# Performance work log

Measured on AMD Instinct MI355X. Metric: run time of the kernel, lower is better.

## Reference

```python
import jax, jax.numpy as jnp
import numpy as np
import math

DIM, HEADS, COMPRESS = 2048, 16, 8
HEAD_DIM = DIM // HEADS          # 128
HALF = HEAD_DIM // 2             # 64 (Q/K head dim after low-rank up-proj)
LATENT = DIM // COMPRESS         # 256
B, S = 2, 2048


def setup_inputs() -> dict:
    key = jax.random.key(0)
    ks = jax.random.split(key, 7)
    sc = lambda fan_in: 1.0 / math.sqrt(fan_in)
    return {
        "x": jax.random.normal(ks[0], (B, S, DIM), jnp.float32),
        "wq_d": jax.random.normal(ks[1], (DIM, LATENT), jnp.float32) * sc(DIM),
        "wkv_d": jax.random.normal(ks[2], (DIM, LATENT), jnp.float32) * sc(DIM),
        "wq_u": jax.random.normal(ks[3], (LATENT, HEADS * HALF), jnp.float32) * sc(LATENT),
        "wk_u": jax.random.normal(ks[4], (LATENT, HEADS * HALF), jnp.float32) * sc(LATENT),
        "wv_u": jax.random.normal(ks[5], (LATENT, DIM), jnp.float32) * sc(LATENT),
        "wo": jax.random.normal(ks[6], (DIM, DIM), jnp.float32) * sc(DIM),
    }


def _rope_tables(seq_len):
    # LlamaRotaryEmbedding with dim = HALF
    inv_freq = 1.0 / (10000.0 ** (jnp.arange(0, HALF, 2, dtype=jnp.float32) / HALF))  # [HALF//2]
    t = jnp.arange(seq_len, dtype=jnp.float32)
    freqs = t[:, None] * inv_freq[None, :]          # [S, HALF//2]
    emb = jnp.concatenate([freqs, freqs], axis=-1)  # [S, HALF]
    cos = jnp.cos(emb)[None, :, None, :]            # [1, S, 1, HALF]
    sin = jnp.sin(emb)[None, :, None, :]
    return cos, sin


def _rotate_half(x):
    x1, x2 = jnp.split(x, 2, axis=-1)
    return jnp.concatenate([-x2, x1], axis=-1)


def reference(x, wq_d, wkv_d, wq_u, wk_u, wv_u, wo):
    b, s, d = x.shape
    q_latent = x @ wq_d                      # [B,S,LATENT]
    kv_latent = x @ wkv_d                    # [B,S,LATENT]
    q = (q_latent @ wq_u).reshape(b, s, HEADS, HALF)
    k = (kv_latent @ wk_u).reshape(b, s, HEADS, HALF)
    v = (kv_latent @ wv_u).reshape(b, s, HEADS, HEAD_DIM)

    cos, sin = _rope_tables(s)
    q = q * cos + _rotate_half(q) * sin
    k = k * cos + _rotate_half(k) * sin

    scale = 1.0 / math.sqrt(HALF)
    attn = jnp.einsum("bqhd,bkhd->bhqk", q, k) * scale   # [B,H,S,S] (no mask, as in source)
    attn = jax.nn.softmax(attn, axis=-1)
    out = jnp.einsum("bhqk,bkhd->bqhd", attn, v)         # [B,S,H,HEAD_DIM]
    out = out.reshape(b, s, d)
    return out @ wo
```

## Files before the change

### kernel.cpp

```cpp
#include <hip/hip_runtime.h>
#include <stdint.h>

typedef unsigned short u16;
typedef __attribute__((ext_vector_type(8))) short bf16x8;
typedef __attribute__((ext_vector_type(4))) float f32x4;
typedef __attribute__((ext_vector_type(4))) unsigned short u16x4;

#define DIM 2048
#define HEADS 16
#define HEAD_DIM 128
#define HALF 64
#define LATENT 256
#define BATCH 2
#define SEQ 2048
#define TOK (BATCH*SEQ)

#if defined(__has_builtin)
#if __has_builtin(__builtin_amdgcn_exp2f)
#define EXP2F(x) __builtin_amdgcn_exp2f(x)
#endif
#endif
#ifndef EXP2F
#define EXP2F(x) exp2f(x)
#endif

#define SCALE_C 0.18033688011112042f

__device__ __forceinline__ u16 f2bf(float f) {
  uint32_t u = __float_as_uint(f);
  u += 0x7fff + ((u >> 16) & 1);
  return (u16)(u >> 16);
}

__device__ __forceinline__ f32x4 mfma16(bf16x8 a, bf16x8 b, f32x4 c) {
  return __builtin_amdgcn_mfma_f32_16x16x32_bf16(a, b, c, 0, 0, 0);
}

__device__ __forceinline__ void async_copy16(const void* g, void* l) {
  __builtin_amdgcn_global_load_lds(
      (const __attribute__((address_space(1))) void*)g,
      (__attribute__((address_space(3))) void*)l, 16, 0, 0);
}

__global__ void prep_k(const float* __restrict__ wq_d, const float* __restrict__ wkv_d,
                       const float* __restrict__ wq_u, const float* __restrict__ wk_u,
                       const float* __restrict__ wv_u, const float* __restrict__ wo,
                       u16* __restrict__ wdT, u16* __restrict__ wquT, u16* __restrict__ wkuT,
                       u16* __restrict__ wvuT, u16* __restrict__ woT,
                       float* __restrict__ ct, float* __restrict__ st) {
  __shared__ float tile[32][33];
  const int f = blockIdx.x;
  const int tx = threadIdx.x, ty = threadIdx.y;

  const float* in = nullptr;
  u16* out = nullptr;
  int N = 0, row_off = 0, out_ld = 0, bx = 0, by = 0;

  if (f < 1024) {
    int z = f >> 9, r = f & 511;
    bx = r & 7; by = r >> 3;
    in = z ? wkv_d : wq_d; out = wdT; row_off = z * 256; N = 256; out_ld = 2048;
  } else if (f < 1536) {
    int r = f - 1024; int z = r >> 8; r &= 255;
    bx = r & 31; by = r >> 5;
    in = z ? wk_u : wq_u; out = z ? wkuT : wquT; row_off = 0; N = 1024; out_ld = 256;
  } else if (f < 2048) {
    int r = f - 1536;
    bx = r & 63; by = r >> 6;
    in = wv_u; out = wvuT; row_off = 0; N = 2048; out_ld = 256;
  } else if (f < 6144) {
    int r = f - 2048;
    bx = r & 63; by = r >> 6;
    in = wo; out = woT; row_off = 0; N = 2048; out_ld = 2048;
  } else {
    int t = (f - 6144) * 256 + ty * 32 + tx;
    int i = t & 31, s = t >> 5;
    float invf = expf(-(float)i * 0.28782313662425575f);
    float a = (float)s * invf;
    ct[t] = cosf(a);
    st[t] = sinf(a);
    return;
  }
  int k0 = by * 32, n0 = bx * 32;
  #pragma unroll
  for (int j = 0; j < 32; j += 8)
    tile[ty + j][tx] = in[(size_t)(k0 + ty + j) * N + n0 + tx];
  __syncthreads();
  #pragma unroll
  for (int j = 0; j < 32; j += 8)
    out[(size_t)(n0 + ty + j + row_off) * out_ld + k0 + tx] = f2bf(tile[tx][ty + j]);
}

template<int NS, int OUTF32>
__global__ void combine_k(const float* __restrict__ p, void* __restrict__ out, int n4, int slab4) {
  int t = blockIdx.x * 256 + threadIdx.x;
  if (t >= n4) return;
  float4 a = ((const float4*)p)[t];
  #pragma unroll
  for (int s = 1; s < NS; ++s) {
    float4 b = ((const float4*)p)[t + (size_t)s * slab4];
    a.x += b.x; a.y += b.y; a.z += b.z; a.w += b.w;
  }
  if (OUTF32) ((float4*)out)[t] = a;
  else { u16x4 o = { f2bf(a.x), f2bf(a.y), f2bf(a.z), f2bf(a.w) };
         *(u16x4*)((u16*)out + (size_t)t * 4) = o; }
}

__global__ __launch_bounds__(256)
void gemm_lat(const float* __restrict__ A, int lda, const u16* __restrict__ BT, int ldb,
              float* __restrict__ Cv, int M, int N, int K) {
  __shared__ __align__(16) u16 As[128 * 32];
  __shared__ __align__(16) u16 Bs[128 * 32];
  const int tid = threadIdx.x;
  const int lane = tid & 63;
  const int wid = tid >> 6;
  const int z = blockIdx.z;
  int koff = z * K;
  const int nb = gridDim.x * gridDim.y;
  int f = blockIdx.x + gridDim.x * blockIdx.y;
  f = (f & 7) * (nb >> 3) + (f >> 3);
  const int m0 = (f / gridDim.x) * 128;
  const int n0 = (f % gridDim.x) * 128;
  const int wr = wid >> 1, wc = wid & 1;
  const int l15 = lane & 15, lg = lane >> 4;
  const int rA = lane >> 2;
  const int kqL = (lane & 3) * 8;
  const int kqS = ((((lane & 3) - ((lane >> 3) & 3)) & 3)) * 8;
  const int sWr = (((lane & 3) + ((lane >> 3) & 3)) & 3) * 8;
  const int rsw = (l15 >> 1) & 3;

  f32x4 acc[4][4] = {};
  const int nk = K / 32;
  for (int kt = 0; kt < nk; ++kt) {
    const int k0 = koff + kt * 32;
    #pragma unroll
    for (int c = 0; c < 2; ++c) {
      int ca = wid * 2 + c;
      const float* ga = A + (size_t)(m0 + ca * 16 + rA) * lda + k0 + kqL;
      float4 v0 = *(const float4*)ga;
      float4 v1 = *(const float4*)(ga + 4);
      union { u16 h[8]; bf16x8 v; } pk;
      pk.h[0] = f2bf(v0.x); pk.h[1] = f2bf(v0.y); pk.h[2] = f2bf(v0.z); pk.h[3] = f2bf(v0.w);
      pk.h[4] = f2bf(v1.x); pk.h[5] = f2bf(v1.y); pk.h[6] = f2bf(v1.z); pk.h[7] = f2bf(v1.w);
      *(bf16x8*)&As[ca * 512 + rA * 32 + sWr] = pk.v;
      const u16* gb = BT + (size_t)(n0 + ca * 16 + rA) * ldb + k0 + kqS;
      async_copy16(gb, &Bs[ca * 512]);
    }
    __syncthreads();
    bf16x8 af[4], bfr[4];
    const int slot = ((lg + rsw) & 3) * 8;
    #pragma unroll
    for (int i = 0; i < 4; ++i) {
      af[i]  = *(const bf16x8*)&As[(wr * 64 + i * 16 + l15) * 32 + slot];
      bfr[i] = *(const bf16x8*)&Bs[(wc * 64 + i * 16 + l15) * 32 + slot];
    }
    #pragma unroll
    for (int i = 0; i < 4; ++i)
      #pragma unroll
      for (int j = 0; j < 4; ++j)
        acc[i][j] = mfma16(af[i], bfr[j], acc[i][j]);
    __syncthreads();
  }
  #pragma unroll
  for (int i = 0; i < 4; ++i) {
    #pragma unroll
    for (int j = 0; j < 4; ++j) {
      int row = m0 + wr * 64 + i * 16 + lg * 4;
      int col = n0 + wc * 64 + j * 16 + l15;
      #pragma unroll
      for (int r = 0; r < 4; ++r)
        Cv[(size_t)z * M * N + (size_t)(row + r) * N + col] = acc[i][j][r];
    }
  }
}

__global__ __launch_bounds__(256)
void gemm_wo(const u16* __restrict__ A, const u16* __restrict__ BT,
             float* __restrict__ C) {
  __shared__ __align__(16) u16 As[3][128 * 32];
  __shared__ __align__(16) u16 Bs[3][128 * 32];
  const int tid = threadIdx.x, lane = tid & 63, wid = tid >> 6;
  const int nb = gridDim.x * gridDim.y;
  int f = blockIdx.x + gridDim.x * blockIdx.y;
  f = (f & 7) * (nb >> 3) + (f >> 3);
  const int m0 = (f / gridDim.x) * 128;
  const int n0 = (f % gridDim.x) * 128;
  const int wr = wid >> 1, wc = wid & 1;
  const int l15 = lane & 15, lg = lane >> 4;
  const int rA = lane >> 2;
  const int kqS = ((((lane & 3) - ((lane >> 3) & 3)) & 3)) * 8;
  const int rsw = (l15 >> 1) & 3;

  f32x4 acc[4][4] = {};

  auto stage = [&](u16* AsD, u16* BsD, int k0) {
    #pragma unroll
    for (int c = 0; c < 2; ++c) {
      int ca = wid * 2 + c;
      async_copy16(A + (size_t)(m0 + ca * 16 + rA) * DIM + k0 + kqS, AsD + ca * 512);
      async_copy16(BT + (size_t)(n0 + ca * 16 + rA) * DIM + k0 + kqS, BsD + ca * 512);
    }
  };
  auto compute = [&](const u16* AsP, const u16* BsP) {
    bf16x8 af[4], bfr[4];
    const int slot = ((lg + rsw) & 3) * 8;
    #pragma unroll
    for (int i = 0; i < 4; ++i) {
      af[i]  = *(const bf16x8*)&AsP[(wr * 64 + i * 16 + l15) * 32 + slot];
      bfr[i] = *(const bf16x8*)&BsP[(wc * 64 + i * 16 + l15) * 32 + slot];
    }
    __builtin_amdgcn_s_setprio(1);
    #pragma unroll
    for (int i = 0; i < 4; ++i)
      #pragma unroll
      for (int j = 0; j < 4; ++j)
        acc[i][j] = mfma16(af[i], bfr[j], acc[i][j]);
    __builtin_amdgcn_s_setprio(0);
  };

#define WAIT4 asm volatile("s_waitcnt vmcnt(4)" ::: "memory")
#define WAIT0 asm volatile("s_waitcnt vmcnt(0)" ::: "memory")
#define BAR   __builtin_amdgcn_s_barrier()

  stage(As[0], Bs[0], 0);
  stage(As[1], Bs[1], 32);
  WAIT4; BAR;
  int t = 0;
  for (int i = 0; i < 20; ++i) {
    stage(As[2], Bs[2], (t + 2) * 32); compute(As[0], Bs[0]); WAIT4; BAR;
    stage(As[0], Bs[0], (t + 3) * 32); compute(As[1], Bs[1]); WAIT4; BAR;
    stage(As[1], Bs[1], (t + 4) * 32); compute(As[2], Bs[2]); WAIT4; BAR;
    t += 3;
  }
  stage(As[2], Bs[2], 62 * 32); compute(As[0], Bs[0]); WAIT4; BAR;
  stage(As[0], Bs[0], 63 * 32); compute(As[1], Bs[1]); WAIT4; BAR;
  compute(As[2], Bs[2]); WAIT0; BAR;
  compute(As[0], Bs[0]);

#undef WAIT4
#undef WAIT0
#undef BAR

  #pragma unroll
  for (int i = 0; i < 4; ++i) {
    #pragma unroll
    for (int j = 0; j < 4; ++j) {
      int row = m0 + wr * 64 + i * 16 + lg * 4;
      int col = n0 + wc * 64 + j * 16 + l15;
      #pragma unroll
      for (int r = 0; r < 4; ++r)
        C[(size_t)(row + r) * DIM + col] = acc[i][j][r];
    }
  }
}

__global__ __launch_bounds__(256)
void upproj_k(const u16* __restrict__ A,
              const u16* __restrict__ wquT, const u16* __restrict__ wkuT,
              const u16* __restrict__ wvuT,
              u16* __restrict__ qb, u16* __restrict__ kb, u16* __restrict__ vT,
              const float* __restrict__ ct, const float* __restrict__ st) {
  __shared__ __align__(16) u16 As[128 * 32];
  __shared__ __align__(16) u16 Bs[128 * 32];
  const int tid = threadIdx.x;
  const int lane = tid & 63;
  const int wid = tid >> 6;
  int f = blockIdx.x;
  f = (f & 7) * 128 + (f >> 3);
  const u16* BT; u16* out; int N, a_off, seg, r;
  if (f < 256)      { seg = 0; r = f;       BT = wquT; out = qb; N = 1024; a_off = 0; }
  else if (f < 512) { seg = 1; r = f - 256; BT = wkuT; out = kb; N = 1024; a_off = 256; }
  else              { seg = 2; r = f - 512; BT = wvuT; out = vT; N = 2048; a_off = 256; }
  const int gx = (seg == 2) ? 16 : 8;
  const int m0 = (r / gx) * 128;
  const int n0 = (r % gx) * 128;
  const int wr = wid >> 1, wc = wid & 1;
  const int l15 = lane & 15, lg = lane >> 4;
  const int rA = lane >> 2;
  const int kqS = ((((lane & 3) - ((lane >> 3) & 3)) & 3)) * 8;
  const int rsw = (l15 >> 1) & 3;

  f32x4 acc[4][4] = {};
  for (int kt = 0; kt < LATENT / 32; ++kt) {
    const int k0 = kt * 32;
    #pragma unroll
    for (int c = 0; c < 2; ++c) {
      int ca = wid * 2 + c;
      async_copy16(A + (size_t)(m0 + ca * 16 + rA) * 512 + a_off + k0 + kqS, &As[ca * 512]);
      async_copy16(BT + (size_t)(n0 + ca * 16 + rA) * LATENT + k0 + kqS, &Bs[ca * 512]);
    }
    __syncthreads();
    bf16x8 af[4], bfr[4];
    const int slot = ((lg + rsw) & 3) * 8;
    #pragma unroll
    for (int i = 0; i < 4; ++i) {
      af[i]  = *(const bf16x8*)&As[(wr * 64 + i * 16 + l15) * 32 + slot];
      bfr[i] = *(const bf16x8*)&Bs[(wc * 64 + i * 16 + l15) * 32 + slot];
    }
    #pragma unroll
    for (int i = 0; i < 4; ++i)
      #pragma unroll
      for (int j = 0; j < 4; ++j)
        acc[i][j] = mfma16(af[i], bfr[j], acc[i][j]);
    __syncthreads();
  }

  if (seg <= 1) {
    const float qs = seg ? 1.0f : SCALE_C;
    #pragma unroll
    for (int i = 0; i < 4; ++i) {
      int rowb = m0 + wr * 64 + i * 16 + lg * 4;
      #pragma unroll
      for (int j = 0; j < 2; ++j) {
        int ii = j * 16 + l15;
        int colb = n0 + wc * 64;
        #pragma unroll
        for (int r2 = 0; r2 < 4; ++r2) {
          int s = (rowb + r2) & (SEQ - 1);
          float c = ct[s * 32 + ii], sn = st[s * 32 + ii];
          float x1 = acc[i][j][r2], x2 = acc[i][j + 2][r2];
          out[(size_t)(rowb + r2) * N + colb + ii]      = f2bf((x1 * c - x2 * sn) * qs);
          out[(size_t)(rowb + r2) * N + colb + ii + 32] = f2bf((x2 * c + x1 * sn) * qs);
        }
      }
    }
  } else {
    const int bb = m0 >> 11;
    #pragma unroll
    for (int i = 0; i < 4; ++i) {
      int rowb = m0 + wr * 64 + i * 16 + lg * 4;
      int s = rowb & (SEQ - 1);
      int pbase = (s & ~31) + (((s & 15) >> 2) << 3) + (((s >> 4) & 1) << 2);
      #pragma unroll
      for (int j = 0; j < 4; ++j) {
        int c = n0 + wc * 64 + j * 16 + l15;
        u16x4 ov = { f2bf(acc[i][j][0]), f2bf(acc[i][j][1]),
                     f2bf(acc[i][j][2]), f2bf(acc[i][j][3]) };
        *(u16x4*)&out[(size_t)bb * SEQ * DIM + (size_t)c * SEQ + pbase] = ov;
      }
    }
  }
}

#define KVB 64
__global__ __launch_bounds__(256, 2)
void attn_kernel(const u16* __restrict__ Q, const u16* __restrict__ Kb,
                 const u16* __restrict__ VT, u16* __restrict__ O) {
  __shared__ __align__(16) u16 Ks[3][KVB * 64];
  __shared__ __align__(16) u16 Vs[3][HEAD_DIM * KVB];

  const int tid = threadIdx.x, lane = tid & 63, wid = tid >> 6;
  int fl = blockIdx.x + 16 * (blockIdx.y + 16 * blockIdx.z);
  fl = (fl & 7) * 64 + (fl >> 3);
  const int q0 = (fl & 15) * 128;
  const int h = (fl >> 4) & 15;
  const int b = fl >> 8;
  const int l15 = lane & 15, lg = lane >> 4;

  const u16* kbp = Kb + (size_t)(b * SEQ) * (HEADS * HALF) + h * HALF;
  const u16* vtb = VT + (size_t)b * SEQ * DIM + (size_t)(h * HEAD_DIM) * SEQ;

  bf16x8 qf[2][2];
  #pragma unroll
  for (int m = 0; m < 2; ++m)
    #pragma unroll
    for (int ks = 0; ks < 2; ++ks)
      qf[m][ks] = *(const bf16x8*)&Q[(size_t)(b * SEQ + q0 + wid * 32 + m * 16 + l15) * (HEADS * HALF)
                                     + h * HALF + ks * 32 + lg * 8];

  f32x4 o[2][8] = {};
  float l_part[2] = {0.f, 0.f};

  const int row8 = lane >> 3;
  const int colB = ((lane & 7) ^ row8) * 16;

  auto stage = [&](u16* KsD, u16* VsD, int kv0) {
    #pragma unroll
    for (int i = 0; i < 2; ++i) {
      int c = wid * 2 + i;
      const u16* src = kbp + (size_t)(kv0 + c * 8 + row8) * (HEADS * HALF) + (colB >> 1);
      async_copy16(src, KsD + c * 512);
    }
    #pragma unroll
    for (int i = 0; i < 4; ++i) {
      int c = wid * 4 + i;
      const u16* src = vtb + (size_t)(c * 8 + row8) * SEQ + kv0 + (colB >> 1);
      async_copy16(src, VsD + c * 512);
    }
  };

  auto compute = [&](const u16* KsP, const u16* VsP) {
    const char* KsB = (const char*)KsP;
    const char* VsB = (const char*)VsP;
    const int kswz = (l15 & 7) << 4;
    bf16x8 kf[2][4];
    #pragma unroll
    for (int ks = 0; ks < 2; ++ks)
      #pragma unroll
      for (int nf = 0; nf < 4; ++nf)
        kf[ks][nf] = *(const bf16x8*)(KsB + (nf * 16 + l15) * 128 + ((ks * 64 + lg * 16) ^ kswz));
    f32x4 s[2][4] = {};
    __builtin_amdgcn_s_setprio(1);
    #pragma unroll
    for (int ks = 0; ks < 2; ++ks)
      #pragma unroll
      for (int nf = 0; nf < 4; ++nf) {
        s[0][nf] = mfma16(kf[ks][nf], qf[0][ks], s[0][nf]);
        s[1][nf] = mfma16(kf[ks][nf], qf[1][ks], s[1][nf]);
      }
    __builtin_amdgcn_s_setprio(0);
    #pragma unroll
    for (int ks2 = 0; ks2 < 2; ++ks2) {
      bf16x8 vf[8];
      #pragma unroll
      for (int db = 0; db < 8; ++db) {
        int row = db * 16 + l15;
        vf[db] = *(const bf16x8*)(VsB + row * 128 + ((ks2 * 64 + lg * 16) ^ ((row & 7) << 4)));
      }
      bf16x8 pa[2];
      #pragma unroll
      for (int m = 0; m < 2; ++m) {
        float p[8];
        #pragma unroll
        for (int nf2 = 0; nf2 < 2; ++nf2)
          #pragma unroll
          for (int r = 0; r < 4; ++r) {
            float v = EXP2F(s[m][ks2 * 2 + nf2][r]);
            p[nf2 * 4 + r] = v;
            l_part[m] += v;
          }
        union { uint32_t u[4]; bf16x8 v8; } pk;
        asm("v_cvt_pk_bf16_f32 %0, %1, %2" : "=v"(pk.u[0]) : "v"(p[0]), "v"(p[1]));
        asm("v_cvt_pk_bf16_f32 %0, %1, %2" : "=v"(pk.u[1]) : "v"(p[2]), "v"(p[3]));
        asm("v_cvt_pk_bf16_f32 %0, %1, %2" : "=v"(pk.u[2]) : "v"(p[4]), "v"(p[5]));
        asm("v_cvt_pk_bf16_f32 %0, %1, %2" : "=v"(pk.u[3]) : "v"(p[6]), "v"(p[7]));
        pa[m] = pk.v8;
      }
      __builtin_amdgcn_s_setprio(1);
      #pragma unroll
      for (int db = 0; db < 8; ++db) {
        o[0][db] = mfma16(pa[0], vf[db], o[0][db]);
        o[1][db] = mfma16(pa[1], vf[db], o[1][db]);
      }
      __builtin_amdgcn_s_setprio(0);
    }
  };

#define WAIT6 asm volatile("s_waitcnt vmcnt(6)" ::: "memory")
#define WAIT0 asm volatile("s_waitcnt vmcnt(0)" ::: "memory")
#define BAR   __builtin_amdgcn_s_barrier()

  stage(Ks[0], Vs[0], 0);
  stage(Ks[1], Vs[1], KVB);
  WAIT6; BAR;
  int t = 0;
  for (int i = 0; i < 10; ++i) {
    stage(Ks[2], Vs[2], (t + 2) * KVB); compute(Ks[0], Vs[0]); WAIT6; BAR;
    stage(Ks[0], Vs[0], (t + 3) * KVB); compute(Ks[1], Vs[1]); WAIT6; BAR;
    stage(Ks[1], Vs[1], (t + 4) * KVB); compute(Ks[2], Vs[2]); WAIT6; BAR;
    t += 3;
  }
  compute(Ks[0], Vs[0]); WAIT0; BAR;
  compute(Ks[1], Vs[1]);

#undef WAIT6
#undef WAIT0
#undef BAR

  #pragma unroll
  for (int m = 0; m < 2; ++m) {
    float l = l_part[m];
    l += __shfl_xor(l, 16);
    l += __shfl_xor(l, 32);
    float inv[4];
    #pragma unroll
    for (int r = 0; r < 4; ++r)
      inv[r] = 1.0f / __shfl(l, lg * 4 + r);
    #pragma unroll
    for (int db = 0; db < 8; ++db)
      #pragma unroll
      for (int r = 0; r < 4; ++r) {
        int row = q0 + wid * 32 + m * 16 + lg * 4 + r;
        O[(size_t)(b * SEQ + row) * DIM + h * HEAD_DIM + db * 16 + l15] = f2bf(o[m][db][r] * inv[r]);
      }
  }
}

extern "C" void kernel_launch(void* const* d_in, const int* in_sizes, int n_in,
                              void* d_out, int out_size, void* d_ws, size_t ws_size,
                              hipStream_t stream) {
  const float* x     = (const float*)d_in[0];
  const float* wq_d  = (const float*)d_in[1];
  const float* wkv_d = (const float*)d_in[2];
  const float* wq_u  = (const float*)d_in[3];
  const float* wk_u  = (const float*)d_in[4];
  const float* wv_u  = (const float*)d_in[5];
  const float* wo    = (const float*)d_in[6];

  char* ws = (char*)d_ws;
  size_t off = 0;
  auto alloc = [&](size_t bytes) -> void* {
    void* p = ws + off;
    off += (bytes + 255) & ~(size_t)255;
    return p;
  };
  u16* wdT    = (u16*)alloc((size_t)512 * DIM * 2);
  u16* wquT   = (u16*)alloc((size_t)1024 * LATENT * 2);
  u16* wkuT   = (u16*)alloc((size_t)1024 * LATENT * 2);
  u16* wvuT   = (u16*)alloc((size_t)DIM * LATENT * 2);
  u16* woT    = (u16*)alloc((size_t)DIM * DIM * 2);
  u16* lat    = (u16*)alloc((size_t)TOK * 512 * 2);
  float* latP = (float*)alloc((size_t)4 * TOK * 512 * 4);
  u16* qb     = (u16*)alloc((size_t)TOK * 1024 * 2);
  u16* kb     = (u16*)alloc((size_t)TOK * 1024 * 2);
  u16* vT     = (u16*)alloc((size_t)TOK * DIM * 2);
  u16* ao     = (u16*)alloc((size_t)TOK * DIM * 2);
  float* ct   = (float*)alloc((size_t)SEQ * 32 * 4);
  float* st   = (float*)alloc((size_t)SEQ * 32 * 4);
  (void)in_sizes; (void)n_in; (void)out_size; (void)ws_size;

  prep_k<<<dim3(6400), dim3(32, 8), 0, stream>>>(wq_d, wkv_d, wq_u, wk_u, wv_u, wo,
                                                 wdT, wquT, wkuT, wvuT, woT, ct, st);

  gemm_lat<<<dim3(4, 32, 4), 256, 0, stream>>>(x, DIM, wdT, DIM, latP, TOK, 512, 512);
  combine_k<4, 0><<<(TOK * 512 / 4 + 255) / 256, 256, 0, stream>>>(latP, lat, TOK * 512 / 4, TOK * 512 / 4);

  upproj_k<<<dim3(1024), 256, 0, stream>>>(lat, wquT, wkuT, wvuT, qb, kb, vT, ct, st);

  attn_kernel<<<dim3(SEQ / 128, HEADS, BATCH), 256, 0, stream>>>(qb, kb, vT, ao);

  gemm_wo<<<dim3(16, 32), 256, 0, stream>>>(ao, woT, (float*)d_out);
}
```

Measured before the change: 157.6 us.

## Store split-K latent partials in bf16 and triple-buffer upproj K loop

The split-K latent GEMM now writes its partial sums as bf16 instead of fp32, and the combine kernel reads and sums bf16 partials eight elements at a time. This halves partial-buffer traffic but adds an extra rounding step before the final sum. The up-projection kernel also gets a 3-stage async LDS pipeline with vmcnt waits, barriers and MFMA priority raising, so global loads overlap compute instead of syncing twice per K step.

```diff
diff --git a/kernel.cpp b/kernel.cpp
--- a/kernel.cpp
+++ b/kernel.cpp
@@ -3,6 +3,7 @@
 
 typedef unsigned short u16;
 typedef __attribute__((ext_vector_type(8))) short bf16x8;
+typedef __attribute__((ext_vector_type(8))) unsigned short u16x8;
 typedef __attribute__((ext_vector_type(4))) float f32x4;
 typedef __attribute__((ext_vector_type(4))) unsigned short u16x4;
 
@@ -30,6 +31,10 @@
   uint32_t u = __float_as_uint(f);
   u += 0x7fff + ((u >> 16) & 1);
   return (u16)(u >> 16);
+}
+
+__device__ __forceinline__ float bf2f(u16 h) {
+  return __uint_as_float((uint32_t)h << 16);
 }
 
 __device__ __forceinline__ f32x4 mfma16(bf16x8 a, bf16x8 b, f32x4 c) {
@@ -91,24 +96,27 @@
     out[(size_t)(n0 + ty + j + row_off) * out_ld + k0 + tx] = f2bf(tile[tx][ty + j]);
 }
 
-template<int NS, int OUTF32>
-__global__ void combine_k(const float* __restrict__ p, void* __restrict__ out, int n4, int slab4) {
+__global__ void combine_bf(const u16* __restrict__ p, u16* __restrict__ out,
+                           int n8, size_t slab) {
   int t = blockIdx.x * 256 + threadIdx.x;
-  if (t >= n4) return;
-  float4 a = ((const float4*)p)[t];
-  #pragma unroll
-  for (int s = 1; s < NS; ++s) {
-    float4 b = ((const float4*)p)[t + (size_t)s * slab4];
-    a.x += b.x; a.y += b.y; a.z += b.z; a.w += b.w;
-  }
-  if (OUTF32) ((float4*)out)[t] = a;
-  else { u16x4 o = { f2bf(a.x), f2bf(a.y), f2bf(a.z), f2bf(a.w) };
-         *(u16x4*)((u16*)out + (size_t)t * 4) = o; }
+  if (t >= n8) return;
+  size_t base = (size_t)t * 8;
+  float a[8] = {};
+  #pragma unroll
+  for (int s = 0; s < 4; ++s) {
+    u16x8 v = *(const u16x8*)&p[base + s * slab];
+    #pragma unroll
+    for (int e = 0; e < 8; ++e) a[e] += bf2f(v[e]);
+  }
+  u16x8 o;
+  #pragma unroll
+  for (int e = 0; e < 8; ++e) o[e] = f2bf(a[e]);
+  *(u16x8*)&out[base] = o;
 }
 
 __global__ __launch_bounds__(256)
 void gemm_lat(const float* __restrict__ A, int lda, const u16* __restrict__ BT, int ldb,
-              float* __restrict__ Cv, int M, int N, int K) {
+              u16* __restrict__ Cv, int M, int N, int K) {
   __shared__ __align__(16) u16 As[128 * 32];
   __shared__ __align__(16) u16 Bs[128 * 32];
   const int tid = threadIdx.x;
@@ -169,7 +177,7 @@
       int col = n0 + wc * 64 + j * 16 + l15;
       #pragma unroll
       for (int r = 0; r < 4; ++r)
-        Cv[(size_t)z * M * N + (size_t)(row + r) * N + col] = acc[i][j][r];
+        Cv[(size_t)z * M * N + (size_t)(row + r) * N + col] = f2bf(acc[i][j][r]);
     }
   }
 }
@@ -260,8 +268,8 @@
               const u16* __restrict__ wvuT,
               u16* __restrict__ qb, u16* __restrict__ kb, u16* __restrict__ vT,
               const float* __restrict__ ct, const float* __restrict__ st) {
-  __shared__ __align__(16) u16 As[128 * 32];
-  __shared__ __align__(16) u16 Bs[128 * 32];
+  __shared__ __align__(16) u16 As[3][128 * 32];
+  __shared__ __align__(16) u16 Bs[3][128 * 32];
   const int tid = threadIdx.x;
   const int lane = tid & 63;
   const int wid = tid >> 6;
@@ -281,29 +289,51 @@
   const int rsw = (l15 >> 1) & 3;
 
   f32x4 acc[4][4] = {};
-  for (int kt = 0; kt < LATENT / 32; ++kt) {
-    const int k0 = kt * 32;
+
+  auto stage = [&](u16* AsD, u16* BsD, int k0) {
     #pragma unroll
     for (int c = 0; c < 2; ++c) {
       int ca = wid * 2 + c;
-      async_copy16(A + (size_t)(m0 + ca * 16 + rA) * 512 + a_off + k0 + kqS, &As[ca * 512]);
-      async_copy16(BT + (size_t)(n0 + ca * 16 + rA) * LATENT + k0 + kqS, &Bs[ca * 512]);
-    }
-    __syncthreads();
+      async_copy16(A + (size_t)(m0 + ca * 16 + rA) * 512 + a_off + k0 + kqS, AsD + ca * 512);
+      async_copy16(BT + (size_t)(n0 + ca * 16 + rA) * LATENT + k0 + kqS, BsD + ca * 512);
+    }
+  };
+  auto compute = [&](const u16* AsP, const u16* BsP) {
     bf16x8 af[4], bfr[4];
     const int slot = ((lg + rsw) & 3) * 8;
     #pragma unroll
     for (int i = 0; i < 4; ++i) {
-      af[i]  = *(const bf16x8*)&As[(wr * 64 + i * 16 + l15) * 32 + slot];
-      bfr[i] = *(const bf16x8*)&Bs[(wc * 64 + i * 16 + l15) * 32 + slot];
-    }
+      af[i]  = *(const bf16x8*)&AsP[(wr * 64 + i * 16 + l15) * 32 + slot];
+      bfr[i] = *(const bf16x8*)&BsP[(wc * 64 + i * 16 + l15) * 32 + slot];
+    }
+    __builtin_amdgcn_s_setprio(1);
     #pragma unroll
     for (int i = 0; i < 4; ++i)
       #pragma unroll
       for (int j = 0; j < 4; ++j)
         acc[i][j] = mfma16(af[i], bfr[j], acc[i][j]);
-    __syncthreads();
-  }
+    __builtin_amdgcn_s_setprio(0);
+  };
+
+#define WAIT4 asm volatile("s_waitcnt vmcnt(4)" ::: "memory")
+#define WAIT0 asm volatile("s_waitcnt vmcnt(0)" ::: "memory")
+#define BAR   __builtin_amdgcn_s_barrier()
+
+  stage(As[0], Bs[0], 0);
+  stage(As[1], Bs[1], 32);
+  WAIT4; BAR;
+  stage(As[2], Bs[2],  64); compute(As[0], Bs[0]); WAIT4; BAR;
+  stage(As[0], Bs[0],  96); compute(As[1], Bs[1]); WAIT4; BAR;
+  stage(As[1], Bs[1], 128); compute(As[2], Bs[2]); WAIT4; BAR;
+  stage(As[2], Bs[2], 160); compute(As[0], Bs[0]); WAIT4; BAR;
+  stage(As[0], Bs[0], 192); compute(As[1], Bs[1]); WAIT4; BAR;
+  stage(As[1], Bs[1], 224); compute(As[2], Bs[2]); WAIT4; BAR;
+  compute(As[0], Bs[0]); WAIT0; BAR;
+  compute(As[1], Bs[1]);
+
+#undef WAIT4
+#undef WAIT0
+#undef BAR
 
   if (seg <= 1) {
     const float qs = seg ? 1.0f : SCALE_C;
@@ -510,7 +540,7 @@
   u16* wvuT   = (u16*)alloc((size_t)DIM * LATENT * 2);
   u16* woT    = (u16*)alloc((size_t)DIM * DIM * 2);
   u16* lat    = (u16*)alloc((size_t)TOK * 512 * 2);
-  float* latP = (float*)alloc((size_t)4 * TOK * 512 * 4);
+  u16* latP   = (u16*)alloc((size_t)4 * TOK * 512 * 2);
   u16* qb     = (u16*)alloc((size_t)TOK * 1024 * 2);
   u16* kb     = (u16*)alloc((size_t)TOK * 1024 * 2);
   u16* vT     = (u16*)alloc((size_t)TOK * DIM * 2);
@@ -523,7 +553,7 @@
                                                  wdT, wquT, wkuT, wvuT, woT, ct, st);
 
   gemm_lat<<<dim3(4, 32, 4), 256, 0, stream>>>(x, DIM, wdT, DIM, latP, TOK, 512, 512);
-  combine_k<4, 0><<<(TOK * 512 / 4 + 255) / 256, 256, 0, stream>>>(latP, lat, TOK * 512 / 4, TOK * 512 / 4);
+  combine_bf<<<(TOK * 512 / 8 + 255) / 256, 256, 0, stream>>>(latP, lat, TOK * 512 / 8, (size_t)TOK * 512);
 
   upproj_k<<<dim3(1024), 256, 0, stream>>>(lat, wquT, wkuT, wvuT, qb, kb, vT, ct, st);
 
```

Measured after the change: 154.8 us. No clear change (-1.8%).
